# Performance work log

Hardware: AMD Instinct MI355X
Metric: run time of the kernel (lower is better)

## Reference

```python
import jax, jax.numpy as jnp
import numpy as np

B, S, CC, CF, E, H, NH = 16, 1024, 8, 8, 64, 1024, 16
DH = H // NH
VOCAB = 10000
EPS = 1e-5


def layer_norm(x, g, b):
    m = x.mean(-1, keepdims=True)
    v = x.var(-1, keepdims=True)
    return (x - m) / jnp.sqrt(v + EPS) * g + b


def setup_inputs():
    key = jax.random.key(0)
    ks = jax.random.split(key, 30)
    f32 = jnp.float32
    n = lambda k, shp, s=0.02: jax.random.normal(k, shp, f32) * s
    inp = {}
    inp['cate_x'] = jax.random.randint(ks[0], (B, S, CC), 0, VOCAB)
    inp['cont_x'] = jax.random.normal(ks[1], (B, S, CF), f32)
    inp['mask'] = jax.random.randint(ks[2], (B, S), 0, 2)
    # parameters
    inp['emb_table'] = n(ks[3], (VOCAB, E)).at[0].set(0.0)  # padding_idx=0
    inp['cate_W'] = n(ks[4], (CC * E, H)); inp['cate_b'] = jnp.zeros((H,), f32)
    inp['cate_ln_g'] = jnp.ones((H,), f32); inp['cate_ln_b'] = jnp.zeros((H,), f32)
    inp['bn_g'] = jnp.ones((CF,), f32); inp['bn_b'] = jnp.zeros((CF,), f32)
    inp['cont_W'] = n(ks[5], (CF, H)); inp['cont_b'] = jnp.zeros((H,), f32)
    inp['cont_ln_g'] = jnp.ones((H,), f32); inp['cont_ln_b'] = jnp.zeros((H,), f32)
    inp['comb_W'] = n(ks[6], (2 * H, H)); inp['comb_b'] = jnp.zeros((H,), f32)
    inp['comb_ln_g'] = jnp.ones((H,), f32); inp['comb_ln_b'] = jnp.zeros((H,), f32)
    inp['Wq'] = n(ks[7], (H, H)); inp['bq'] = jnp.zeros((H,), f32)
    inp['Wk'] = n(ks[8], (H, H)); inp['bk'] = jnp.zeros((H,), f32)
    inp['Wv'] = n(ks[9], (H, H)); inp['bv'] = jnp.zeros((H,), f32)
    inp['Wo'] = n(ks[10], (H, H)); inp['bo'] = jnp.zeros((H,), f32)
    return inp


def reference(cate_x, cont_x, mask, emb_table, cate_W, cate_b, cate_ln_g, cate_ln_b,
              bn_g, bn_b, cont_W, cont_b, cont_ln_g, cont_ln_b,
              comb_W, comb_b, comb_ln_g, comb_ln_b,
              Wq, bq, Wk, bk, Wv, bv, Wo, bo):
    # categorical path: embed -> flatten cols -> Linear+LN
    cate_emb = emb_table[cate_x].reshape(B, S, CC * E)
    cate_h = layer_norm(cate_emb @ cate_W + cate_b, cate_ln_g, cate_ln_b)
    # continuous path: BatchNorm1d over flattened (B*S, CF) with batch stats
    xf = cont_x.reshape(-1, CF)
    mu = xf.mean(0)
    var = xf.var(0)  # biased, as torch BN normalization
    xn = ((xf - mu) / jnp.sqrt(var + EPS) * bn_g + bn_b).reshape(B, S, CF)
    cont_h = layer_norm(xn @ cont_W + cont_b, cont_ln_g, cont_ln_b)
    # combine: ReLU -> Linear -> LN
    seq = jax.nn.relu(jnp.concatenate([cate_h, cont_h], axis=2))
    x = layer_norm(seq @ comb_W + comb_b, comb_ln_g, comb_ln_b)  # [B,S,H]
    # multi-head attention (dropout is identity in eval)
    Q = (x @ Wq + bq).reshape(B, S, NH, DH)
    K = (x @ Wk + bk).reshape(B, S, NH, DH)
    V = (x @ Wv + bv).reshape(B, S, NH, DH)
    scores = jnp.einsum('bqhd,bkhd->bhqk', Q, K) / np.sqrt(DH).astype(np.float32)
    # faithful to source: mask broadcast over the QUERY axis
    scores = jnp.where(mask[:, None, :, None] == 0, -1e7, scores)
    attn = jax.nn.softmax(scores, axis=-1)
    out = jnp.einsum('bhqk,bkhd->bqhd', attn, V).reshape(B, S, H)
    out = out @ Wo + bo
    return out[:, -1:, -1]  # [B,1]
```

## Files before the change

kernel.cpp:

```cpp
#include <hip/hip_runtime.h>
#include <hip/hip_bf16.h>
#include <math.h>

#define EPS 1e-5f

typedef unsigned short u16;
typedef __attribute__((ext_vector_type(8))) short bf16x8;
typedef __attribute__((ext_vector_type(4))) float f32x4;

__device__ __forceinline__ float b2f(u16 u) {
  union { unsigned int i; float f; } v; v.i = ((unsigned int)u) << 16; return v.f;
}
__device__ __forceinline__ u16 f2b(float f) {
  union { float f; unsigned int i; } v; v.f = f;
  unsigned int r = v.i + 0x7fff + ((v.i >> 16) & 1);
  return (u16)(r >> 16);
}

__device__ __forceinline__ void gload_lds16(const u16* g, u16* l) {
  __builtin_amdgcn_global_load_lds(
      (const __attribute__((address_space(1))) unsigned int*)g,
      (__attribute__((address_space(3))) unsigned int*)l, 16, 0, 0);
}

__global__ __launch_bounds__(256) void prep_k(
    const float* __restrict__ cx, float* __restrict__ part_bn,
    float* __restrict__ outacc,
    const float* __restrict__ emb, u16* __restrict__ embb,
    const float* __restrict__ cate_W, u16* __restrict__ cateWT) {
  __shared__ float shmem[64 * 65];
  const int bid = blockIdx.x, tid = threadIdx.x;

  if (bid == 0) {
    if (tid < 16) outacc[tid] = 0.f;
    return;
  }
  if (bid <= 64) {
    int pb = bid - 1;
    int gid = pb * 256 + tid;
    float4 a = ((const float4*)cx)[2 * gid];
    float4 b = ((const float4*)cx)[2 * gid + 1];
    float v[16];
    v[0] = a.x; v[1] = a.y; v[2] = a.z; v[3] = a.w;
    v[4] = b.x; v[5] = b.y; v[6] = b.z; v[7] = b.w;
#pragma unroll
    for (int i = 0; i < 8; ++i) v[8 + i] = v[i] * v[i];
#pragma unroll
    for (int off = 32; off; off >>= 1)
#pragma unroll
      for (int i = 0; i < 16; ++i) v[i] += __shfl_down(v[i], off);
    int l = tid & 63, wv_ = tid >> 6;
    if (l == 0)
#pragma unroll
      for (int i = 0; i < 16; ++i) shmem[wv_ * 16 + i] = v[i];
    __syncthreads();
    if (tid < 16)
      part_bn[pb * 16 + tid] = shmem[tid] + shmem[16 + tid] + shmem[32 + tid] + shmem[48 + tid];
    return;
  }
  if (bid <= 689) {
    int i = (bid - 65) * 256 + tid;
    if (i < 160000) {
      float4 v = ((const float4*)emb)[i];
      ushort4 u; u.x = f2b(v.x); u.y = f2b(v.y); u.z = f2b(v.z); u.w = f2b(v.w);
      ((ushort4*)embb)[i] = u;
    }
    return;
  }
  {
    int local = bid - 690;
    int n0 = (local & 15) * 64, k0 = (local >> 4) * 64;
    int c = tid & 63, r0 = tid >> 6;
#pragma unroll
    for (int i = 0; i < 16; ++i) {
      int r = r0 + i * 4;
      shmem[r * 65 + c] = cate_W[(size_t)(k0 + r) * 1024 + n0 + c];
    }
    __syncthreads();
#pragma unroll
    for (int i = 0; i < 16; ++i) {
      int r = r0 + i * 4;
      cateWT[(size_t)(n0 + r) * 512 + k0 + c] = f2b(shmem[c * 65 + r]);
    }
  }
}

template <int MODE>
__global__ __launch_bounds__(512) void gemm256(
    const u16* __restrict__ A0, const u16* __restrict__ A1,
    const int* __restrict__ idx, const u16* __restrict__ embb,
    const u16* __restrict__ BT, const float* __restrict__ bias,
    u16* __restrict__ C, int K) {
  __shared__ u16 As[2][2][8192];
  __shared__ u16 Bs[2][2][8192];
  __shared__ int sidx[MODE == 1 ? 2048 : 4];
  const int tid = threadIdx.x;
  const int bid = blockIdx.x;
  const int chunk = gridDim.x >> 3;
  const int swz = (bid & 7) * chunk + (bid >> 3);
  const int row0 = (swz >> 2) * 256;
  const int col0 = (swz & 3) * 256;

  const int rr8 = tid >> 3;
  const int p8  = tid & 7;
  const int sl  = p8 ^ (rr8 & 7);

  const int l   = tid & 63;
  const int w   = tid >> 6;
  const int wrh = w >> 2;
  const int wcq = w & 3;
  const int hb  = wcq >> 1;
  const int rbb = (wcq & 1) * 64;
  const int lr  = l & 15;
  const int lk  = l >> 4;

  f32x4 acc[8][4];
#pragma unroll
  for (int m = 0; m < 8; ++m)
#pragma unroll
    for (int n = 0; n < 4; ++n) acc[m][n] = (f32x4){0.f, 0.f, 0.f, 0.f};

  const int nt = K >> 6;
  const int nit = nt >> 1;

  if (MODE == 1) {
    *(int4*)&sidx[tid * 4] = *(const int4*)&idx[row0 * 8 + tid * 4];
    __syncthreads();
  }

  auto stageA = [&](int t, int h) {
    const int k0 = t << 6;
    const int buf = t & 1;
#pragma unroll
    for (int i = 0; i < 2; ++i) {
      const u16* asrc;
      if (MODE == 1) {
        int id = sidx[(h * 128 + i * 64 + rr8) * 8 + (k0 >> 6)];
        asrc = embb + (size_t)id * 64 + sl * 8;
      } else {
        int ar = row0 + h * 128 + i * 64 + rr8;
        const u16* base = (k0 < 1024) ? A0 : A1;
        asrc = base + (size_t)ar * 1024 + (k0 & 1023) + sl * 8;
      }
      gload_lds16(asrc, &As[buf][h][i * 4096 + tid * 8]);
    }
  };
  auto stageB = [&](int t, int h) {
    const int k0 = t << 6;
    const int buf = t & 1;
#pragma unroll
    for (int i = 0; i < 2; ++i) {
      int br = col0 + h * 128 + i * 64 + rr8;
      gload_lds16(BT + (size_t)br * K + k0 + sl * 8,
                  &Bs[buf][h][i * 4096 + tid * 8]);
    }
  };

  bf16x8 bfr[4][2];
  auto loadB = [&](int buf) {
#pragma unroll
    for (int n = 0; n < 4; ++n)
#pragma unroll
      for (int ks = 0; ks < 2; ++ks) {
        int rowb = rbb + n * 16 + lr;
        int ph = (ks * 4 + lk) ^ (lr & 7);
        bfr[n][ks] = *(const bf16x8*)&Bs[buf][hb][rowb * 64 + ph * 8];
      }
  };
  auto loadA = [&](bf16x8 (&af)[2][2], int buf, int q) {
#pragma unroll
    for (int mm = 0; mm < 2; ++mm)
#pragma unroll
      for (int ks = 0; ks < 2; ++ks) {
        int rowa = (q * 2 + mm) * 16 + lr;
        int ph = (ks * 4 + lk) ^ (lr & 7);
        af[mm][ks] = *(const bf16x8*)&As[buf][wrh][rowa * 64 + ph * 8];
      }
  };
  auto mfma_quad = [&](bf16x8 (&af)[2][2], int q) {
    __builtin_amdgcn_s_setprio(1);
#pragma unroll
    for (int ks = 0; ks < 2; ++ks)
#pragma unroll
      for (int mm = 0; mm < 2; ++mm)
#pragma unroll
        for (int n = 0; n < 4; ++n)
          acc[q * 2 + mm][n] = __builtin_amdgcn_mfma_f32_16x16x32_bf16(
              af[mm][ks], bfr[n][ks], acc[q * 2 + mm][n], 0, 0, 0);
    __builtin_amdgcn_s_setprio(0);
  };

  stageA(0, 0); stageA(0, 1);
  stageB(0, 0); stageB(0, 1);
  stageB(1, 0); stageB(1, 1);
  asm volatile("s_waitcnt vmcnt(4)" ::: "memory");
  __builtin_amdgcn_s_barrier();

  for (int it = 0; it < nit; ++it) {
    const int T = it * 2;
    const bool more = (T + 2 < nt);
    bf16x8 af[2][2];

    loadB(0); loadA(af, 0, 0);
    stageA(T + 1, 0);
    __builtin_amdgcn_s_barrier();
    asm volatile("s_waitcnt lgkmcnt(0)" ::: "memory");
    mfma_quad(af, 0);
    __builtin_amdgcn_s_barrier();
    loadA(af, 0, 1);
    stageA(T + 1, 1);
    __builtin_amdgcn_s_barrier();
    asm volatile("s_waitcnt lgkmcnt(0)" ::: "memory");
    mfma_quad(af, 1);
    __builtin_amdgcn_s_barrier();
    loadA(af, 0, 2);
    if (more) stageB(T + 2, 0);
    __builtin_amdgcn_s_barrier();
    asm volatile("s_waitcnt lgkmcnt(0)" ::: "memory");
    mfma_quad(af, 2);
    __builtin_amdgcn_s_barrier();
    loadA(af, 0, 3);
    if (more) stageB(T + 2, 1);
    __builtin_amdgcn_s_barrier();
    asm volatile("s_waitcnt lgkmcnt(0)" ::: "memory");
    mfma_quad(af, 3);
    if (more) asm volatile("s_waitcnt vmcnt(4)" ::: "memory");
    else      asm volatile("s_waitcnt vmcnt(0)" ::: "memory");
    __builtin_amdgcn_s_barrier();

    loadB(1); loadA(af, 1, 0);
    if (more) stageA(T + 2, 0);
    __builtin_amdgcn_s_barrier();
    asm volatile("s_waitcnt lgkmcnt(0)" ::: "memory");
    mfma_quad(af, 0);
    __builtin_amdgcn_s_barrier();
    loadA(af, 1, 1);
    if (more) stageA(T + 2, 1);
    __builtin_amdgcn_s_barrier();
    asm volatile("s_waitcnt lgkmcnt(0)" ::: "memory");
    mfma_quad(af, 1);
    __builtin_amdgcn_s_barrier();
    loadA(af, 1, 2);
    if (more) stageB(T + 3, 0);
    __builtin_amdgcn_s_barrier();
    asm volatile("s_waitcnt lgkmcnt(0)" ::: "memory");
    mfma_quad(af, 2);
    __builtin_amdgcn_s_barrier();
    loadA(af, 1, 3);
    if (more) stageB(T + 3, 1);
    __builtin_amdgcn_s_barrier();
    asm volatile("s_waitcnt lgkmcnt(0)" ::: "memory");
    mfma_quad(af, 3);
    if (it + 1 < nit) {
      asm volatile("s_waitcnt vmcnt(4)" ::: "memory");
      __builtin_amdgcn_s_barrier();
    }
  }

  float bv_[4];
#pragma unroll
  for (int n = 0; n < 4; ++n) bv_[n] = bias[col0 + wcq * 64 + n * 16 + lr];
#pragma unroll
  for (int m = 0; m < 8; ++m) {
#pragma unroll
    for (int n = 0; n < 4; ++n) {
      int cc = col0 + wcq * 64 + n * 16 + lr;
#pragma unroll
      for (int q4 = 0; q4 < 4; ++q4) {
        int rr = row0 + wrh * 128 + m * 16 + lk * 4 + q4;
        C[(size_t)rr * 1024 + cc] = f2b(acc[m][n][q4] + bv_[n]);
      }
    }
  }
}

__device__ __forceinline__ void ln_body(u16* __restrict__ buf,
                                        const float* __restrict__ g,
                                        const float* __restrict__ b, int relu,
                                        int blk, int tid) {
  int lane = tid & 63, wave = tid >> 6;
  size_t row = (size_t)blk * 4 + wave;
  u16* p = buf + row * 1024 + lane * 16;
  uint4 u0 = *(uint4*)p;
  uint4 u1 = *(uint4*)(p + 8);
  float x[16];
#pragma unroll
  for (int i = 0; i < 4; ++i) {
    unsigned int w0 = ((unsigned int*)&u0)[i];
    unsigned int w1 = ((unsigned int*)&u1)[i];
    x[2 * i]     = b2f((u16)(w0 & 0xffff));
    x[2 * i + 1] = b2f((u16)(w0 >> 16));
    x[8 + 2 * i]     = b2f((u16)(w1 & 0xffff));
    x[8 + 2 * i + 1] = b2f((u16)(w1 >> 16));
  }
  float s = 0.f, s2 = 0.f;
#pragma unroll
  for (int i = 0; i < 16; ++i) { s += x[i]; s2 += x[i] * x[i]; }
#pragma unroll
  for (int off = 32; off; off >>= 1) { s += __shfl_xor(s, off); s2 += __shfl_xor(s2, off); }
  float mean = s * (1.f / 1024.f);
  float var = s2 * (1.f / 1024.f) - mean * mean;
  float rs = rsqrtf(var + EPS);
  float y[16];
#pragma unroll
  for (int q = 0; q < 4; ++q) {
    float4 gv = *(const float4*)(g + lane * 16 + q * 4);
    float4 bv = *(const float4*)(b + lane * 16 + q * 4);
    y[4 * q]     = (x[4 * q]     - mean) * rs * gv.x + bv.x;
    y[4 * q + 1] = (x[4 * q + 1] - mean) * rs * gv.y + bv.y;
    y[4 * q + 2] = (x[4 * q + 2] - mean) * rs * gv.z + bv.z;
    y[4 * q + 3] = (x[4 * q + 3] - mean) * rs * gv.w + bv.w;
  }
  if (relu)
#pragma unroll
    for (int i = 0; i < 16; ++i) y[i] = fmaxf(y[i], 0.f);
  uint4 o0, o1;
#pragma unroll
  for (int i = 0; i < 4; ++i) {
    ((unsigned int*)&o0)[i] = (unsigned int)f2b(y[2 * i]) | ((unsigned int)f2b(y[2 * i + 1]) << 16);
    ((unsigned int*)&o1)[i] = (unsigned int)f2b(y[8 + 2 * i]) | ((unsigned int)f2b(y[8 + 2 * i + 1]) << 16);
  }
  *(uint4*)p = o0;
  *(uint4*)(p + 8) = o1;
}

__global__ __launch_bounds__(256) void ln_k(u16* __restrict__ buf,
                                            const float* __restrict__ g,
                                            const float* __restrict__ b, int relu) {
  ln_body(buf, g, b, relu, blockIdx.x, threadIdx.x);
}

__device__ __forceinline__ void cont_body(const float* __restrict__ cx,
                                          const float* __restrict__ part_bn,
                                          const float* __restrict__ bn_g,
                                          const float* __restrict__ bn_b,
                                          const float* __restrict__ W,
                                          const float* __restrict__ cb,
                                          const float* __restrict__ g,
                                          const float* __restrict__ bb,
                                          u16* __restrict__ out,
                                          int row0, int tid) {
  __shared__ float sp[4][16];
  __shared__ float tt[16];
  __shared__ float ab[2][8];
  __shared__ float xn[8][8];
  __shared__ float rr1[4][8], rr2[4][8];

  if (tid < 64) {
    int f = tid & 15, qd = tid >> 4;
    float s = 0.f;
    for (int j = qd * 16; j < qd * 16 + 16; ++j) s += part_bn[j * 16 + f];
    sp[qd][f] = s;
  }
  __syncthreads();
  if (tid < 16) tt[tid] = sp[0][tid] + sp[1][tid] + sp[2][tid] + sp[3][tid];
  __syncthreads();
  if (tid < 8) {
    float mu = tt[tid] * (1.f / 16384.f);
    float var = tt[8 + tid] * (1.f / 16384.f) - mu * mu;
    float a = rsqrtf(var + EPS) * bn_g[tid];
    ab[0][tid] = a;
    ab[1][tid] = bn_b[tid] - mu * a;
  }
  __syncthreads();
  if (tid < 64) {
    int r = tid >> 3, f = tid & 7;
    xn[r][f] = ab[0][f] * cx[(row0 + r) * 8 + f] + ab[1][f];
  }
  __syncthreads();

  int c = tid * 4;
  float4 cbv = *(const float4*)(cb + c);
  float acc[8][4];
#pragma unroll
  for (int r = 0; r < 8; ++r) {
    acc[r][0] = cbv.x; acc[r][1] = cbv.y; acc[r][2] = cbv.z; acc[r][3] = cbv.w;
  }
  for (int k = 0; k < 8; ++k) {
    float4 w4 = *(const float4*)(W + k * 1024 + c);
#pragma unroll
    for (int r = 0; r < 8; ++r) {
      float xv = xn[r][k];
      acc[r][0] = fmaf(xv, w4.x, acc[r][0]);
      acc[r][1] = fmaf(xv, w4.y, acc[r][1]);
      acc[r][2] = fmaf(xv, w4.z, acc[r][2]);
      acc[r][3] = fmaf(xv, w4.w, acc[r][3]);
    }
  }
  float s1[8], s2[8];
#pragma unroll
  for (int r = 0; r < 8; ++r) {
    s1[r] = acc[r][0] + acc[r][1] + acc[r][2] + acc[r][3];
    s2[r] = acc[r][0] * acc[r][0] + acc[r][1] * acc[r][1] +
            acc[r][2] * acc[r][2] + acc[r][3] * acc[r][3];
  }
#pragma unroll
  for (int off = 32; off; off >>= 1)
#pragma unroll
    for (int r = 0; r < 8; ++r) {
      s1[r] += __shfl_down(s1[r], off);
      s2[r] += __shfl_down(s2[r], off);
    }
  int lane = tid & 63, wv = tid >> 6;
  if (lane == 0)
#pragma unroll
    for (int r = 0; r < 8; ++r) { rr1[wv][r] = s1[r]; rr2[wv][r] = s2[r]; }
  __syncthreads();
  float4 gv = *(const float4*)(g + c);
  float4 bv = *(const float4*)(bb + c);
#pragma unroll
  for (int r = 0; r < 8; ++r) {
    float ss = rr1[0][r] + rr1[1][r] + rr1[2][r] + rr1[3][r];
    float qq = rr2[0][r] + rr2[1][r] + rr2[2][r] + rr2[3][r];
    float mean = ss * (1.f / 1024.f);
    float var = qq * (1.f / 1024.f) - mean * mean;
    float rs = rsqrtf(var + EPS);
    float y0 = fmaxf((acc[r][0] - mean) * rs * gv.x + bv.x, 0.f);
    float y1 = fmaxf((acc[r][1] - mean) * rs * gv.y + bv.y, 0.f);
    float y2 = fmaxf((acc[r][2] - mean) * rs * gv.z + bv.z, 0.f);
    float y3 = fmaxf((acc[r][3] - mean) * rs * gv.w + bv.w, 0.f);
    ushort4 o; o.x = f2b(y0); o.y = f2b(y1); o.z = f2b(y2); o.w = f2b(y3);
    *(ushort4*)(out + (size_t)(row0 + r) * 1024 + c) = o;
  }
}

__global__ __launch_bounds__(256) void mid_k(
    u16* __restrict__ X1, const float* __restrict__ cate_g,
    const float* __restrict__ cate_bb,
    const float* __restrict__ comb_W, u16* __restrict__ combWT,
    const float* __restrict__ Wv, const float* __restrict__ Wo,
    u16* __restrict__ wvob_hi, u16* __restrict__ wvob_lo,
    float* __restrict__ woc,
    const float* __restrict__ cx, const float* __restrict__ part_bn,
    const float* __restrict__ bn_g, const float* __restrict__ bn_b,
    const float* __restrict__ cont_W, const float* __restrict__ cont_b,
    const float* __restrict__ cont_g, const float* __restrict__ cont_bb,
    u16* __restrict__ X2) {
  __shared__ float shmem[64 * 65];
  const int bid = blockIdx.x, tid = threadIdx.x;
  if (bid < 4096) {
    ln_body(X1, cate_g, cate_bb, 1, bid, tid);
    return;
  }
  if (bid < 4608) {
    int local = bid - 4096;
    int n0 = (local & 15) * 64, k0 = (local >> 4) * 64;
    int c = tid & 63, r0 = tid >> 6;
#pragma unroll
    for (int i = 0; i < 16; ++i) {
      int r = r0 + i * 4;
      shmem[r * 65 + c] = comb_W[(size_t)(k0 + r) * 1024 + n0 + c];
    }
    __syncthreads();
#pragma unroll
    for (int i = 0; i < 16; ++i) {
      int r = r0 + i * 4;
      combWT[(size_t)(n0 + r) * 2048 + k0 + c] = f2b(shmem[c * 65 + r]);
    }
    return;
  }
  if (bid < 4672) {
    int local = bid - 4608;
    int h = local >> 2, jc = local & 3;
    if (tid < 64) shmem[tid] = Wo[(size_t)(h * 64 + tid) * 1024 + 1023];
    __syncthreads();
    if (jc == 0 && tid < 64) woc[h * 64 + tid] = shmem[tid];
    int j = jc * 256 + tid;
    const float* vr = Wv + (size_t)j * 1024 + h * 64;
    float s = 0.f;
    for (int d4 = 0; d4 < 64; d4 += 4) {
      float4 w4 = *(const float4*)(vr + d4);
      s = fmaf(w4.x, shmem[d4], s);
      s = fmaf(w4.y, shmem[d4 + 1], s);
      s = fmaf(w4.z, shmem[d4 + 2], s);
      s = fmaf(w4.w, shmem[d4 + 3], s);
    }
    u16 hi = f2b(s);
    float lo = s - b2f(hi);
    wvob_hi[h * 1024 + j] = hi;
    wvob_lo[h * 1024 + j] = f2b(lo);
    return;
  }
  {
    int row0 = (bid - 4672) * 8;
    cont_body(cx, part_bn, bn_g, bn_b, cont_W, cont_b, cont_g, cont_bb, X2,
              row0, tid);
  }
}

__global__ __launch_bounds__(256) void qproj_k(const u16* __restrict__ x,
                                               const float* __restrict__ Wq,
                                               const float* __restrict__ bq,
                                               float* __restrict__ q) {
  __shared__ u16 xs[16][1024];
  __shared__ float part[16][16][16];
  int tid = threadIdx.x;
  for (int i = tid; i < 4096; i += 256) {
    int b = i >> 8, off = (i & 255) * 4;
    *(ushort4*)&xs[b][off] =
        *(const ushort4*)(x + ((size_t)(b * 1024 + 1023)) * 1024 + off);
  }
  __syncthreads();
  int c = tid & 15;
  int col = blockIdx.x * 16 + c;
  int kq = tid >> 4;
  float acc[16];
#pragma unroll
  for (int b = 0; b < 16; ++b) acc[b] = 0.f;
  for (int k = kq * 64; k < kq * 64 + 64; ++k) {
    float wv = Wq[(size_t)k * 1024 + col];
#pragma unroll
    for (int b = 0; b < 16; ++b) acc[b] = fmaf(b2f(xs[b][k]), wv, acc[b]);
  }
#pragma unroll
  for (int b = 0; b < 16; ++b) part[kq][b][c] = acc[b];
  __syncthreads();
  if (tid < 256) {
    int b = tid >> 4, cc = tid & 15;
    float s = 0.f;
#pragma unroll
    for (int j = 0; j < 16; ++j) s += part[j][b][cc];
    q[b * 1024 + blockIdx.x * 16 + cc] = s + bq[blockIdx.x * 16 + cc];
  }
}

__global__ __launch_bounds__(256) void kq_k(const float* __restrict__ Wk,
                                            const float* __restrict__ bk,
                                            const float* __restrict__ q,
                                            u16* __restrict__ qtb,
                                            float* __restrict__ bkq) {
  int h = blockIdx.x >> 2, jc = blockIdx.x & 3;
  int tid = threadIdx.x;
  __shared__ float Qs[16][64];
  for (int i = tid; i < 1024; i += 256) {
    int b = i >> 6, d = i & 63;
    Qs[b][d] = q[b * 1024 + h * 64 + d];
  }
  __syncthreads();
  int j = jc * 256 + tid;
  float acc[16];
#pragma unroll
  for (int b = 0; b < 16; ++b) acc[b] = 0.f;
  const float* wr = Wk + (size_t)j * 1024 + h * 64;
  for (int d4 = 0; d4 < 64; d4 += 4) {
    float4 w4 = *(const float4*)(wr + d4);
#pragma unroll
    for (int b = 0; b < 16; ++b) {
      acc[b] = fmaf(w4.x, Qs[b][d4], acc[b]);
      acc[b] = fmaf(w4.y, Qs[b][d4 + 1], acc[b]);
      acc[b] = fmaf(w4.z, Qs[b][d4 + 2], acc[b]);
      acc[b] = fmaf(w4.w, Qs[b][d4 + 3], acc[b]);
    }
  }
#pragma unroll
  for (int b = 0; b < 16; ++b) qtb[((size_t)b * 16 + h) * 1024 + j] = f2b(acc[b]);
  if (jc == 0 && tid < 16) {
    int b = tid;
    float s = 0.f;
    for (int d = 0; d < 64; ++d) s = fmaf(bk[h * 64 + d], Qs[b][d], s);
    bkq[b * 16 + h] = s;
  }
}

__global__ __launch_bounds__(256) void score_k(const u16* __restrict__ x,
                                               const u16* __restrict__ qtb,
                                               const float* __restrict__ bkq,
                                               const int* __restrict__ mask,
                                               const u16* __restrict__ whi,
                                               const u16* __restrict__ wlo,
                                               float* __restrict__ sc,
                                               float* __restrict__ y) {
  int b = blockIdx.x >> 4, kc = blockIdx.x & 15;
  int tid = threadIdx.x;
  int l = tid & 63, w = tid >> 6;
  int keybase = kc * 64 + w * 16;
  int lr = l & 15, ls = l >> 4;
  int masked = (mask[b * 1024 + 1023] == 0);

  f32x4 acc = (f32x4){0.f, 0.f, 0.f, 0.f};
  f32x4 acy = (f32x4){0.f, 0.f, 0.f, 0.f};
  const u16* xb = x + (size_t)b * 1024 * 1024;
  const u16* qb = qtb + (size_t)b * 16 * 1024;
  for (int k0 = 0; k0 < 1024; k0 += 32) {
    bf16x8 bfr = *(const bf16x8*)&qb[(size_t)lr * 1024 + k0 + ls * 8];
    bf16x8 bh  = *(const bf16x8*)&whi[(size_t)lr * 1024 + k0 + ls * 8];
    bf16x8 bl  = *(const bf16x8*)&wlo[(size_t)lr * 1024 + k0 + ls * 8];
    bf16x8 afr = *(const bf16x8*)&xb[(size_t)(keybase + lr) * 1024 + k0 + ls * 8];
    acc = __builtin_amdgcn_mfma_f32_16x16x32_bf16(afr, bfr, acc, 0, 0, 0);
    acy = __builtin_amdgcn_mfma_f32_16x16x32_bf16(afr, bh, acy, 0, 0, 0);
    acy = __builtin_amdgcn_mfma_f32_16x16x32_bf16(afr, bl, acy, 0, 0, 0);
  }
  int h = lr;
  float bq_ = bkq[b * 16 + h];
#pragma unroll
  for (int q = 0; q < 4; ++q) {
    int key = keybase + ls * 4 + q;
    float v = masked ? 0.f : (acc[q] + bq_) * 0.125f;
    sc[((size_t)b * 16 + h) * 1024 + key] = v;
    y[((size_t)b * 16 + h) * 1024 + key] = acy[q];
  }
}

__global__ __launch_bounds__(256) void fin_k(const float* __restrict__ sc,
                                             const float* __restrict__ y,
                                             float* __restrict__ outacc) {
  int bh = blockIdx.x, tid = threadIdx.x;
  float4 v = ((const float4*)(sc + (size_t)bh * 1024))[tid];
  float m = fmaxf(fmaxf(v.x, v.y), fmaxf(v.z, v.w));
#pragma unroll
  for (int off = 32; off; off >>= 1) m = fmaxf(m, __shfl_down(m, off));
  __shared__ float rm[4], rs_[4], rd_[4];
  int lane = tid & 63, wv = tid >> 6;
  if (lane == 0) rm[wv] = m;
  __syncthreads();
  m = fmaxf(fmaxf(rm[0], rm[1]), fmaxf(rm[2], rm[3]));
  float e0 = expf(v.x - m), e1 = expf(v.y - m), e2 = expf(v.z - m), e3 = expf(v.w - m);
  float4 yv = ((const float4*)(y + (size_t)bh * 1024))[tid];
  float s = e0 + e1 + e2 + e3;
  float d = e0 * yv.x + e1 * yv.y + e2 * yv.z + e3 * yv.w;
#pragma unroll
  for (int off = 32; off; off >>= 1) {
    s += __shfl_down(s, off);
    d += __shfl_down(d, off);
  }
  if (lane == 0) { rs_[wv] = s; rd_[wv] = d; }
  __syncthreads();
  if (tid == 0) {
    float Z = rs_[0] + rs_[1] + rs_[2] + rs_[3];
    float D = rd_[0] + rd_[1] + rd_[2] + rd_[3];
    atomicAdd(&outacc[bh >> 4], D / Z);
  }
}

__global__ __launch_bounds__(256) void bfinal_k(const float* __restrict__ outacc,
                                                const float* __restrict__ bv,
                                                const float* __restrict__ woc,
                                                const float* __restrict__ bo,
                                                float* __restrict__ out) {
  int tid = threadIdx.x;
  float s = 0.f;
  for (int i = tid; i < 1024; i += 256) s = fmaf(bv[i], woc[i], s);
#pragma unroll
  for (int off = 32; off; off >>= 1) s += __shfl_down(s, off);
  __shared__ float r[4];
  int lane = tid & 63, wv = tid >> 6;
  if (lane == 0) r[wv] = s;
  __syncthreads();
  float bc = r[0] + r[1] + r[2] + r[3] + bo[1023];
  if (tid < 16) out[tid] = outacc[tid] + bc;
}

extern "C" void kernel_launch(void* const* d_in, const int* in_sizes, int n_in,
                              void* d_out, int out_size, void* d_ws, size_t ws_size,
                              hipStream_t stream) {
  const int*   cate_x  = (const int*)d_in[0];
  const float* cont_x  = (const float*)d_in[1];
  const int*   mask    = (const int*)d_in[2];
  const float* emb     = (const float*)d_in[3];
  const float* cate_W  = (const float*)d_in[4];
  const float* cate_b  = (const float*)d_in[5];
  const float* cate_g  = (const float*)d_in[6];
  const float* cate_bb = (const float*)d_in[7];
  const float* bn_g    = (const float*)d_in[8];
  const float* bn_b    = (const float*)d_in[9];
  const float* cont_W  = (const float*)d_in[10];
  const float* cont_b  = (const float*)d_in[11];
  const float* cont_g  = (const float*)d_in[12];
  const float* cont_bb = (const float*)d_in[13];
  const float* Wq = (const float*)d_in[18]; const float* bq = (const float*)d_in[19];
  const float* Wk = (const float*)d_in[20]; const float* bk = (const float*)d_in[21];
  const float* Wv = (const float*)d_in[22]; const float* bv = (const float*)d_in[23];
  const float* Wo = (const float*)d_in[24]; const float* bo = (const float*)d_in[25];
  const float* comb_W  = (const float*)d_in[14];
  const float* comb_b  = (const float*)d_in[15];
  const float* comb_g  = (const float*)d_in[16];
  const float* comb_bb = (const float*)d_in[17];
  float* out = (float*)d_out;

  char* w = (char*)d_ws;
  float* stats   = (float*)w;
  float* outacc  = stats + 16;
  float* part_bn = (float*)(w + 256);
  float* qbuf    = (float*)(w + 8192);
  u16* embb      = (u16*)(w + 131328);
  u16* cateWT    = (u16*)(w + 1411328);
  u16* combWT    = (u16*)(w + 2459904);
  float* sc      = (float*)(w + 6654208);
  u16*   qtb     = (u16*)(w + 7702784);
  float* bkq     = (float*)(w + 8292608);
  float* ybuf    = (float*)(w + 8388608);
  u16* wvob_hi   = (u16*)(w + 9437184);
  u16* wvob_lo   = (u16*)(w + 9469952);
  float* woc     = (float*)(w + 9502720);
  u16* X1        = (u16*)(w + 10848512);
  u16* X2        = X1 + (size_t)16777216;
  u16* xb        = X2 + (size_t)16777216;

  prep_k<<<818, 256, 0, stream>>>(cont_x, part_bn, outacc, emb, embb,
                                  cate_W, cateWT);

  gemm256<1><<<256, 512, 0, stream>>>(nullptr, nullptr, cate_x, embb, cateWT,
                                      cate_b, X1, 512);
  mid_k<<<6720, 256, 0, stream>>>(X1, cate_g, cate_bb, comb_W, combWT, Wv, Wo,
                                  wvob_hi, wvob_lo, woc, cont_x, part_bn, bn_g,
                                  bn_b, cont_W, cont_b, cont_g, cont_bb, X2);
  gemm256<2><<<256, 512, 0, stream>>>(X1, X2, nullptr, nullptr, combWT,
                                      comb_b, xb, 2048);
  ln_k<<<4096, 256, 0, stream>>>(xb, comb_g, comb_bb, 0);

  qproj_k<<<64, 256, 0, stream>>>(xb, Wq, bq, qbuf);
  kq_k<<<64, 256, 0, stream>>>(Wk, bk, qbuf, qtb, bkq);
  score_k<<<256, 256, 0, stream>>>(xb, qtb, bkq, mask, wvob_hi, wvob_lo, sc, ybuf);
  fin_k<<<256, 256, 0, stream>>>(sc, ybuf, outacc);
  bfinal_k<<<1, 256, 0, stream>>>(outacc, bv, woc, bo, out);
}
```

Measured before the change: 198.7 us.

## Fuse attention tail kernels into one cooperative kernel with grid syncs

The five small tail kernels (q projection, K·q, score MFMA, softmax finalize, bias final) are merged into a single cooperative kernel of 256 blocks, with grid.sync() between stages. This removes four kernel launch boundaries and their inter-kernel gaps on a tail that is latency-dominated. In exchange it adds grid-wide barrier costs and a cooperative launch, and the combined shared memory (~45KB per block) may limit residency.

Result: slower. 297.7 us (+49.8%).

```diff
diff --git a/kernel.cpp b/kernel.cpp
--- a/kernel.cpp
+++ b/kernel.cpp
@@ -1,6 +1,9 @@
 #include <hip/hip_runtime.h>
 #include <hip/hip_bf16.h>
+#include <hip/hip_cooperative_groups.h>
 #include <math.h>
+
+namespace cg = cooperative_groups;
 
 #define EPS 1e-5f
 
@@ -488,166 +491,163 @@
   }
 }
 
-__global__ __launch_bounds__(256) void qproj_k(const u16* __restrict__ x,
-                                               const float* __restrict__ Wq,
-                                               const float* __restrict__ bq,
-                                               float* __restrict__ q) {
-  __shared__ u16 xs[16][1024];
-  __shared__ float part[16][16][16];
-  int tid = threadIdx.x;
-  for (int i = tid; i < 4096; i += 256) {
-    int b = i >> 8, off = (i & 255) * 4;
-    *(ushort4*)&xs[b][off] =
-        *(const ushort4*)(x + ((size_t)(b * 1024 + 1023)) * 1024 + off);
-  }
-  __syncthreads();
-  int c = tid & 15;
-  int col = blockIdx.x * 16 + c;
-  int kq = tid >> 4;
-  float acc[16];
-#pragma unroll
-  for (int b = 0; b < 16; ++b) acc[b] = 0.f;
-  for (int k = kq * 64; k < kq * 64 + 64; ++k) {
-    float wv = Wq[(size_t)k * 1024 + col];
-#pragma unroll
-    for (int b = 0; b < 16; ++b) acc[b] = fmaf(b2f(xs[b][k]), wv, acc[b]);
-  }
-#pragma unroll
-  for (int b = 0; b < 16; ++b) part[kq][b][c] = acc[b];
-  __syncthreads();
-  if (tid < 256) {
-    int b = tid >> 4, cc = tid & 15;
+__global__ __launch_bounds__(256) void tail_k(
+    const u16* __restrict__ x,
+    const float* __restrict__ Wq, const float* __restrict__ bq,
+    float* __restrict__ q,
+    const float* __restrict__ Wk, const float* __restrict__ bk,
+    u16* __restrict__ qtb, float* __restrict__ bkq,
+    const int* __restrict__ mask,
+    const u16* __restrict__ whi, const u16* __restrict__ wlo,
+    float* __restrict__ sc, float* __restrict__ y,
+    float* __restrict__ outacc,
+    const float* __restrict__ bv, const float* __restrict__ woc,
+    const float* __restrict__ bo, float* __restrict__ out) {
+  cg::grid_group grid = cg::this_grid();
+  const int bid = blockIdx.x, tid = threadIdx.x;
+
+  if (bid < 64) {
+    __shared__ u16 xs[16][1024];
+    __shared__ float part[16][16][16];
+    for (int i = tid; i < 4096; i += 256) {
+      int b = i >> 8, off = (i & 255) * 4;
+      *(ushort4*)&xs[b][off] =
+          *(const ushort4*)(x + ((size_t)(b * 1024 + 1023)) * 1024 + off);
+    }
+    __syncthreads();
+    int c = tid & 15;
+    int col = bid * 16 + c;
+    int kq = tid >> 4;
+    float acc[16];
+#pragma unroll
+    for (int b = 0; b < 16; ++b) acc[b] = 0.f;
+    for (int k = kq * 64; k < kq * 64 + 64; ++k) {
+      float wv = Wq[(size_t)k * 1024 + col];
+#pragma unroll
+      for (int b = 0; b < 16; ++b) acc[b] = fmaf(b2f(xs[b][k]), wv, acc[b]);
+    }
+#pragma unroll
+    for (int b = 0; b < 16; ++b) part[kq][b][c] = acc[b];
+    __syncthreads();
+    {
+      int b = tid >> 4, cc = tid & 15;
+      float s = 0.f;
+#pragma unroll
+      for (int j = 0; j < 16; ++j) s += part[j][b][cc];
+      q[b * 1024 + bid * 16 + cc] = s + bq[bid * 16 + cc];
+    }
+  }
+  grid.sync();
+
+  if (bid < 64) {
+    int h = bid >> 2, jc = bid & 3;
+    __shared__ float Qs[16][64];
+    for (int i = tid; i < 1024; i += 256) {
+      int b = i >> 6, d = i & 63;
+      Qs[b][d] = q[b * 1024 + h * 64 + d];
+    }
+    __syncthreads();
+    int j = jc * 256 + tid;
+    float acc[16];
+#pragma unroll
+    for (int b = 0; b < 16; ++b) acc[b] = 0.f;
+    const float* wr = Wk + (size_t)j * 1024 + h * 64;
+    for (int d4 = 0; d4 < 64; d4 += 4) {
+      float4 w4 = *(const float4*)(wr + d4);
+#pragma unroll
+      for (int b = 0; b < 16; ++b) {
+        acc[b] = fmaf(w4.x, Qs[b][d4], acc[b]);
+        acc[b] = fmaf(w4.y, Qs[b][d4 + 1], acc[b]);
+        acc[b] = fmaf(w4.z, Qs[b][d4 + 2], acc[b]);
+        acc[b] = fmaf(w4.w, Qs[b][d4 + 3], acc[b]);
+      }
+    }
+#pragma unroll
+    for (int b = 0; b < 16; ++b) qtb[((size_t)b * 16 + h) * 1024 + j] = f2b(acc[b]);
+    if (jc == 0 && tid < 16) {
+      int b = tid;
+      float s = 0.f;
+      for (int d = 0; d < 64; ++d) s = fmaf(bk[h * 64 + d], Qs[b][d], s);
+      bkq[b * 16 + h] = s;
+    }
+  }
+  grid.sync();
+
+  {
+    int b = bid >> 4, kc = bid & 15;
+    int l = tid & 63, w = tid >> 6;
+    int keybase = kc * 64 + w * 16;
+    int lr = l & 15, ls = l >> 4;
+    int masked = (mask[b * 1024 + 1023] == 0);
+
+    f32x4 acc = (f32x4){0.f, 0.f, 0.f, 0.f};
+    f32x4 acy = (f32x4){0.f, 0.f, 0.f, 0.f};
+    const u16* xb = x + (size_t)b * 1024 * 1024;
+    const u16* qb = qtb + (size_t)b * 16 * 1024;
+    for (int k0 = 0; k0 < 1024; k0 += 32) {
+      bf16x8 bfr = *(const bf16x8*)&qb[(size_t)lr * 1024 + k0 + ls * 8];
+      bf16x8 bh  = *(const bf16x8*)&whi[(size_t)lr * 1024 + k0 + ls * 8];
+      bf16x8 bl  = *(const bf16x8*)&wlo[(size_t)lr * 1024 + k0 + ls * 8];
+      bf16x8 afr = *(const bf16x8*)&xb[(size_t)(keybase + lr) * 1024 + k0 + ls * 8];
+      acc = __builtin_amdgcn_mfma_f32_16x16x32_bf16(afr, bfr, acc, 0, 0, 0);
+      acy = __builtin_amdgcn_mfma_f32_16x16x32_bf16(afr, bh, acy, 0, 0, 0);
+      acy = __builtin_amdgcn_mfma_f32_16x16x32_bf16(afr, bl, acy, 0, 0, 0);
+    }
+    int h = lr;
+    float bq_ = bkq[b * 16 + h];
+#pragma unroll
+    for (int qq = 0; qq < 4; ++qq) {
+      int key = keybase + ls * 4 + qq;
+      float v = masked ? 0.f : (acc[qq] + bq_) * 0.125f;
+      sc[((size_t)b * 16 + h) * 1024 + key] = v;
+      y[((size_t)b * 16 + h) * 1024 + key] = acy[qq];
+    }
+  }
+  grid.sync();
+
+  {
+    int bh = bid;
+    float4 v = ((const float4*)(sc + (size_t)bh * 1024))[tid];
+    float m = fmaxf(fmaxf(v.x, v.y), fmaxf(v.z, v.w));
+#pragma unroll
+    for (int off = 32; off; off >>= 1) m = fmaxf(m, __shfl_down(m, off));
+    __shared__ float rm[4], rs_[4], rd_[4];
+    int lane = tid & 63, wv = tid >> 6;
+    if (lane == 0) rm[wv] = m;
+    __syncthreads();
+    m = fmaxf(fmaxf(rm[0], rm[1]), fmaxf(rm[2], rm[3]));
+    float e0 = expf(v.x - m), e1 = expf(v.y - m);
+    float e2 = expf(v.z - m), e3 = expf(v.w - m);
+    float4 yv = ((const float4*)(y + (size_t)bh * 1024))[tid];
+    float s = e0 + e1 + e2 + e3;
+    float d = e0 * yv.x + e1 * yv.y + e2 * yv.z + e3 * yv.w;
+#pragma unroll
+    for (int off = 32; off; off >>= 1) {
+      s += __shfl_down(s, off);
+      d += __shfl_down(d, off);
+    }
+    if (lane == 0) { rs_[wv] = s; rd_[wv] = d; }
+    __syncthreads();
+    if (tid == 0) {
+      float Z = rs_[0] + rs_[1] + rs_[2] + rs_[3];
+      float D = rd_[0] + rd_[1] + rd_[2] + rd_[3];
+      atomicAdd(&outacc[bh >> 4], D / Z);
+    }
+  }
+  grid.sync();
+
+  if (bid == 0) {
     float s = 0.f;
-#pragma unroll
-    for (int j = 0; j < 16; ++j) s += part[j][b][cc];
-    q[b * 1024 + blockIdx.x * 16 + cc] = s + bq[blockIdx.x * 16 + cc];
-  }
-}
-
-__global__ __launch_bounds__(256) void kq_k(const float* __restrict__ Wk,
-                                            const float* __restrict__ bk,
-                                            const float* __restrict__ q,
-                                            u16* __restrict__ qtb,
-                                            float* __restrict__ bkq) {
-  int h = blockIdx.x >> 2, jc = blockIdx.x & 3;
-  int tid = threadIdx.x;
-  __shared__ float Qs[16][64];
-  for (int i = tid; i < 1024; i += 256) {
-    int b = i >> 6, d = i & 63;
-    Qs[b][d] = q[b * 1024 + h * 64 + d];
-  }
-  __syncthreads();
-  int j = jc * 256 + tid;
-  float acc[16];
-#pragma unroll
-  for (int b = 0; b < 16; ++b) acc[b] = 0.f;
-  const float* wr = Wk + (size_t)j * 1024 + h * 64;
-  for (int d4 = 0; d4 < 64; d4 += 4) {
-    float4 w4 = *(const float4*)(wr + d4);
-#pragma unroll
-    for (int b = 0; b < 16; ++b) {
-      acc[b] = fmaf(w4.x, Qs[b][d4], acc[b]);
-      acc[b] = fmaf(w4.y, Qs[b][d4 + 1], acc[b]);
-      acc[b] = fmaf(w4.z, Qs[b][d4 + 2], acc[b]);
-      acc[b] = fmaf(w4.w, Qs[b][d4 + 3], acc[b]);
-    }
-  }
-#pragma unroll
-  for (int b = 0; b < 16; ++b) qtb[((size_t)b * 16 + h) * 1024 + j] = f2b(acc[b]);
-  if (jc == 0 && tid < 16) {
-    int b = tid;
-    float s = 0.f;
-    for (int d = 0; d < 64; ++d) s = fmaf(bk[h * 64 + d], Qs[b][d], s);
-    bkq[b * 16 + h] = s;
-  }
-}
-
-__global__ __launch_bounds__(256) void score_k(const u16* __restrict__ x,
-                                               const u16* __restrict__ qtb,
-                                               const float* __restrict__ bkq,
-                                               const int* __restrict__ mask,
-                                               const u16* __restrict__ whi,
-                                               const u16* __restrict__ wlo,
-                                               float* __restrict__ sc,
-                                               float* __restrict__ y) {
-  int b = blockIdx.x >> 4, kc = blockIdx.x & 15;
-  int tid = threadIdx.x;
-  int l = tid & 63, w = tid >> 6;
-  int keybase = kc * 64 + w * 16;
-  int lr = l & 15, ls = l >> 4;
-  int masked = (mask[b * 1024 + 1023] == 0);
-
-  f32x4 acc = (f32x4){0.f, 0.f, 0.f, 0.f};
-  f32x4 acy = (f32x4){0.f, 0.f, 0.f, 0.f};
-  const u16* xb = x + (size_t)b * 1024 * 1024;
-  const u16* qb = qtb + (size_t)b * 16 * 1024;
-  for (int k0 = 0; k0 < 1024; k0 += 32) {
-    bf16x8 bfr = *(const bf16x8*)&qb[(size_t)lr * 1024 + k0 + ls * 8];
-    bf16x8 bh  = *(const bf16x8*)&whi[(size_t)lr * 1024 + k0 + ls * 8];
-    bf16x8 bl  = *(const bf16x8*)&wlo[(size_t)lr * 1024 + k0 + ls * 8];
-    bf16x8 afr = *(const bf16x8*)&xb[(size_t)(keybase + lr) * 1024 + k0 + ls * 8];
-    acc = __builtin_amdgcn_mfma_f32_16x16x32_bf16(afr, bfr, acc, 0, 0, 0);
-    acy = __builtin_amdgcn_mfma_f32_16x16x32_bf16(afr, bh, acy, 0, 0, 0);
-    acy = __builtin_amdgcn_mfma_f32_16x16x32_bf16(afr, bl, acy, 0, 0, 0);
-  }
-  int h = lr;
-  float bq_ = bkq[b * 16 + h];
-#pragma unroll
-  for (int q = 0; q < 4; ++q) {
-    int key = keybase + ls * 4 + q;
-    float v = masked ? 0.f : (acc[q] + bq_) * 0.125f;
-    sc[((size_t)b * 16 + h) * 1024 + key] = v;
-    y[((size_t)b * 16 + h) * 1024 + key] = acy[q];
-  }
-}
-
-__global__ __launch_bounds__(256) void fin_k(const float* __restrict__ sc,
-                                             const float* __restrict__ y,
-                                             float* __restrict__ outacc) {
-  int bh = blockIdx.x, tid = threadIdx.x;
-  float4 v = ((const float4*)(sc + (size_t)bh * 1024))[tid];
-  float m = fmaxf(fmaxf(v.x, v.y), fmaxf(v.z, v.w));
-#pragma unroll
-  for (int off = 32; off; off >>= 1) m = fmaxf(m, __shfl_down(m, off));
-  __shared__ float rm[4], rs_[4], rd_[4];
-  int lane = tid & 63, wv = tid >> 6;
-  if (lane == 0) rm[wv] = m;
-  __syncthreads();
-  m = fmaxf(fmaxf(rm[0], rm[1]), fmaxf(rm[2], rm[3]));
-  float e0 = expf(v.x - m), e1 = expf(v.y - m), e2 = expf(v.z - m), e3 = expf(v.w - m);
-  float4 yv = ((const float4*)(y + (size_t)bh * 1024))[tid];
-  float s = e0 + e1 + e2 + e3;
-  float d = e0 * yv.x + e1 * yv.y + e2 * yv.z + e3 * yv.w;
-#pragma unroll
-  for (int off = 32; off; off >>= 1) {
-    s += __shfl_down(s, off);
-    d += __shfl_down(d, off);
-  }
-  if (lane == 0) { rs_[wv] = s; rd_[wv] = d; }
-  __syncthreads();
-  if (tid == 0) {
-    float Z = rs_[0] + rs_[1] + rs_[2] + rs_[3];
-    float D = rd_[0] + rd_[1] + rd_[2] + rd_[3];
-    atomicAdd(&outacc[bh >> 4], D / Z);
-  }
-}
-
-__global__ __launch_bounds__(256) void bfinal_k(const float* __restrict__ outacc,
-                                                const float* __restrict__ bv,
-                                                const float* __restrict__ woc,
-                                                const float* __restrict__ bo,
-                                                float* __restrict__ out) {
-  int tid = threadIdx.x;
-  float s = 0.f;
-  for (int i = tid; i < 1024; i += 256) s = fmaf(bv[i], woc[i], s);
-#pragma unroll
-  for (int off = 32; off; off >>= 1) s += __shfl_down(s, off);
-  __shared__ float r[4];
-  int lane = tid & 63, wv = tid >> 6;
-  if (lane == 0) r[wv] = s;
-  __syncthreads();
-  float bc = r[0] + r[1] + r[2] + r[3] + bo[1023];
-  if (tid < 16) out[tid] = outacc[tid] + bc;
+    for (int i = tid; i < 1024; i += 256) s = fmaf(bv[i], woc[i], s);
+#pragma unroll
+    for (int off = 32; off; off >>= 1) s += __shfl_down(s, off);
+    __shared__ float r[4];
+    int lane = tid & 63, wv = tid >> 6;
+    if (lane == 0) r[wv] = s;
+    __syncthreads();
+    float bc = r[0] + r[1] + r[2] + r[3] + bo[1023];
+    if (tid < 16) out[tid] = outacc[tid] + bc;
+  }
 }
 
 extern "C" void kernel_launch(void* const* d_in, const int* in_sizes, int n_in,
@@ -708,9 +708,15 @@
                                       comb_b, xb, 2048);
   ln_k<<<4096, 256, 0, stream>>>(xb, comb_g, comb_bb, 0);
 
-  qproj_k<<<64, 256, 0, stream>>>(xb, Wq, bq, qbuf);
-  kq_k<<<64, 256, 0, stream>>>(Wk, bk, qbuf, qtb, bkq);
-  score_k<<<256, 256, 0, stream>>>(xb, qtb, bkq, mask, wvob_hi, wvob_lo, sc, ybuf);
-  fin_k<<<256, 256, 0, stream>>>(sc, ybuf, outacc);
-  bfinal_k<<<1, 256, 0, stream>>>(outacc, bv, woc, bo, out);
-}
+  {
+    const u16* xcb = xb;
+    void* targs[] = {
+        (void*)&xcb, (void*)&Wq, (void*)&bq, (void*)&qbuf,
+        (void*)&Wk, (void*)&bk, (void*)&qtb, (void*)&bkq,
+        (void*)&mask, (void*)&wvob_hi, (void*)&wvob_lo,
+        (void*)&sc, (void*)&ybuf, (void*)&outacc,
+        (void*)&bv, (void*)&woc, (void*)&bo, (void*)&out};
+    hipLaunchCooperativeKernel((const void*)tail_k, dim3(256), dim3(256),
+                               targs, 0, stream);
+  }
+}
```

## Fold final LayerNorm into downstream projections via per-row stats from GEMM epilogue

Applied to the files above, without the earlier changes.

The standalone comb LayerNorm pass over the 16M-element xb buffer is removed. The comb GEMM epilogue now emits per-row partial sums and sums of squares, and a small kernel turns them into mean and rstd. Gamma and beta are folded algebraically into the K-side query vectors and the V·Wo weights, and correction terms are applied per key in score_k. This removes one full read-modify-write of the activation buffer and a launch, at the cost of extra reductions, atomics and some precision risk from computing variance as E[x²]-mean² on bf16 outputs.

Result: faster. 192.4 us (-3.2%).

```diff
diff --git a/kernel.cpp b/kernel.cpp
--- a/kernel.cpp
+++ b/kernel.cpp
@@ -25,7 +25,7 @@
 
 __global__ __launch_bounds__(256) void prep_k(
     const float* __restrict__ cx, float* __restrict__ part_bn,
-    float* __restrict__ outacc,
+    float* __restrict__ outacc, float* __restrict__ Sall,
     const float* __restrict__ emb, u16* __restrict__ embb,
     const float* __restrict__ cate_W, u16* __restrict__ cateWT) {
   __shared__ float shmem[64 * 65];
@@ -33,6 +33,7 @@
 
   if (bid == 0) {
     if (tid < 16) outacc[tid] = 0.f;
+    for (int i = tid; i < 544; i += 256) Sall[i] = 0.f;
     return;
   }
   if (bid <= 64) {
@@ -90,7 +91,7 @@
     const u16* __restrict__ A0, const u16* __restrict__ A1,
     const int* __restrict__ idx, const u16* __restrict__ embb,
     const u16* __restrict__ BT, const float* __restrict__ bias,
-    u16* __restrict__ C, int K) {
+    u16* __restrict__ C, int K, float* __restrict__ pstat) {
   __shared__ u16 As[2][2][8192];
   __shared__ u16 Bs[2][2][8192];
   __shared__ int sidx[MODE == 1 ? 2048 : 4];
@@ -272,6 +273,54 @@
       }
     }
   }
+
+  if (MODE == 2) {
+    __syncthreads();
+    float* sst = (float*)&As[0][0][0];
+#pragma unroll
+    for (int m = 0; m < 8; ++m) {
+#pragma unroll
+      for (int q4 = 0; q4 < 4; ++q4) {
+        float p1 = 0.f, p2 = 0.f;
+#pragma unroll
+        for (int n = 0; n < 4; ++n) {
+          float v = acc[m][n][q4] + bv_[n];
+          p1 += v; p2 += v * v;
+        }
+#pragma unroll
+        for (int off = 1; off < 16; off <<= 1) {
+          p1 += __shfl_xor(p1, off);
+          p2 += __shfl_xor(p2, off);
+        }
+        if (lr == 0) {
+          int rl = wrh * 128 + m * 16 + lk * 4 + q4;
+          sst[(rl * 4 + wcq) * 2 + 0] = p1;
+          sst[(rl * 4 + wcq) * 2 + 1] = p2;
+        }
+      }
+    }
+    __syncthreads();
+    if (tid < 256) {
+      int rl = tid;
+      float s1 = sst[rl * 8] + sst[rl * 8 + 2] + sst[rl * 8 + 4] + sst[rl * 8 + 6];
+      float s2 = sst[rl * 8 + 1] + sst[rl * 8 + 3] + sst[rl * 8 + 5] + sst[rl * 8 + 7];
+      size_t row = (size_t)(row0 + rl);
+      pstat[(row * 4 + (col0 >> 8)) * 2 + 0] = s1;
+      pstat[(row * 4 + (col0 >> 8)) * 2 + 1] = s2;
+    }
+  }
+}
+
+__global__ __launch_bounds__(256) void stat_k(const float* __restrict__ pstat,
+                                              float* __restrict__ stats) {
+  int row = blockIdx.x * 256 + threadIdx.x;
+  const float* p = pstat + (size_t)row * 8;
+  float s1 = p[0] + p[2] + p[4] + p[6];
+  float s2 = p[1] + p[3] + p[5] + p[7];
+  float mean = s1 * (1.f / 1024.f);
+  float var = s2 * (1.f / 1024.f) - mean * mean;
+  stats[row * 2] = mean;
+  stats[row * 2 + 1] = rsqrtf(var + EPS);
 }
 
 __device__ __forceinline__ void ln_body(u16* __restrict__ buf,
@@ -322,12 +371,6 @@
   }
   *(uint4*)p = o0;
   *(uint4*)(p + 8) = o1;
-}
-
-__global__ __launch_bounds__(256) void ln_k(u16* __restrict__ buf,
-                                            const float* __restrict__ g,
-                                            const float* __restrict__ b, int relu) {
-  ln_body(buf, g, b, relu, blockIdx.x, threadIdx.x);
 }
 
 __device__ __forceinline__ void cont_body(const float* __restrict__ cx,
@@ -429,8 +472,9 @@
     const float* __restrict__ cate_bb,
     const float* __restrict__ comb_W, u16* __restrict__ combWT,
     const float* __restrict__ Wv, const float* __restrict__ Wo,
+    const float* __restrict__ comb_g, const float* __restrict__ comb_bbv,
     u16* __restrict__ wvob_hi, u16* __restrict__ wvob_lo,
-    float* __restrict__ woc,
+    float* __restrict__ woc, float* __restrict__ Swg, float* __restrict__ Swb,
     const float* __restrict__ cx, const float* __restrict__ part_bn,
     const float* __restrict__ bn_g, const float* __restrict__ bn_b,
     const float* __restrict__ cont_W, const float* __restrict__ cont_b,
@@ -475,10 +519,25 @@
       s = fmaf(w4.z, shmem[d4 + 2], s);
       s = fmaf(w4.w, shmem[d4 + 3], s);
     }
-    u16 hi = f2b(s);
-    float lo = s - b2f(hi);
+    float sg_ = s * comb_g[j];
+    u16 hi = f2b(sg_);
+    float lo = sg_ - b2f(hi);
     wvob_hi[h * 1024 + j] = hi;
     wvob_lo[h * 1024 + j] = f2b(lo);
+    float swgp = sg_;
+    float swbp = s * comb_bbv[j];
+#pragma unroll
+    for (int off = 32; off; off >>= 1) {
+      swgp += __shfl_down(swgp, off);
+      swbp += __shfl_down(swbp, off);
+    }
+    int lane = tid & 63, wv = tid >> 6;
+    if (lane == 0) { shmem[64 + wv] = swgp; shmem[68 + wv] = swbp; }
+    __syncthreads();
+    if (tid == 0) {
+      atomicAdd(&Swg[h], shmem[64] + shmem[65] + shmem[66] + shmem[67]);
+      atomicAdd(&Swb[h], shmem[68] + shmem[69] + shmem[70] + shmem[71]);
+    }
     return;
   }
   {
@@ -489,16 +548,35 @@
 }
 
 __global__ __launch_bounds__(256) void qproj_k(const u16* __restrict__ x,
+                                               const float* __restrict__ stats,
+                                               const float* __restrict__ g,
+                                               const float* __restrict__ bb,
                                                const float* __restrict__ Wq,
                                                const float* __restrict__ bq,
                                                float* __restrict__ q) {
   __shared__ u16 xs[16][1024];
   __shared__ float part[16][16][16];
+  __shared__ float sm[16], sr[16];
   int tid = threadIdx.x;
+  if (tid < 16) {
+    size_t row = (size_t)tid * 1024 + 1023;
+    sm[tid] = stats[row * 2];
+    sr[tid] = stats[row * 2 + 1];
+  }
+  __syncthreads();
   for (int i = tid; i < 4096; i += 256) {
     int b = i >> 8, off = (i & 255) * 4;
-    *(ushort4*)&xs[b][off] =
+    ushort4 u =
         *(const ushort4*)(x + ((size_t)(b * 1024 + 1023)) * 1024 + off);
+    float4 gv = *(const float4*)(g + off);
+    float4 bv = *(const float4*)(bb + off);
+    float m = sm[b], r = sr[b];
+    ushort4 o;
+    o.x = f2b((b2f(u.x) - m) * r * gv.x + bv.x);
+    o.y = f2b((b2f(u.y) - m) * r * gv.y + bv.y);
+    o.z = f2b((b2f(u.z) - m) * r * gv.z + bv.z);
+    o.w = f2b((b2f(u.w) - m) * r * gv.w + bv.w);
+    *(ushort4*)&xs[b][off] = o;
   }
   __syncthreads();
   int c = tid & 15;
@@ -515,7 +593,7 @@
 #pragma unroll
   for (int b = 0; b < 16; ++b) part[kq][b][c] = acc[b];
   __syncthreads();
-  if (tid < 256) {
+  {
     int b = tid >> 4, cc = tid & 15;
     float s = 0.f;
 #pragma unroll
@@ -527,11 +605,16 @@
 __global__ __launch_bounds__(256) void kq_k(const float* __restrict__ Wk,
                                             const float* __restrict__ bk,
                                             const float* __restrict__ q,
+                                            const float* __restrict__ g,
+                                            const float* __restrict__ bb,
                                             u16* __restrict__ qtb,
-                                            float* __restrict__ bkq) {
+                                            float* __restrict__ bkq,
+                                            float* __restrict__ Sg,
+                                            float* __restrict__ Sb) {
   int h = blockIdx.x >> 2, jc = blockIdx.x & 3;
   int tid = threadIdx.x;
   __shared__ float Qs[16][64];
+  __shared__ float rg[4][16], rb[4][16];
   for (int i = tid; i < 1024; i += 256) {
     int b = i >> 6, d = i & 63;
     Qs[b][d] = q[b * 1024 + h * 64 + d];
@@ -552,8 +635,32 @@
       acc[b] = fmaf(w4.w, Qs[b][d4 + 3], acc[b]);
     }
   }
-#pragma unroll
-  for (int b = 0; b < 16; ++b) qtb[((size_t)b * 16 + h) * 1024 + j] = f2b(acc[b]);
+  float gj = g[j], bbj = bb[j];
+  float sgp[16], sbp[16];
+#pragma unroll
+  for (int b = 0; b < 16; ++b) {
+    u16 qg = f2b(acc[b] * gj);
+    qtb[((size_t)b * 16 + h) * 1024 + j] = qg;
+    sgp[b] = b2f(qg);
+    sbp[b] = acc[b] * bbj;
+  }
+#pragma unroll
+  for (int off = 32; off; off >>= 1)
+#pragma unroll
+    for (int b = 0; b < 16; ++b) {
+      sgp[b] += __shfl_down(sgp[b], off);
+      sbp[b] += __shfl_down(sbp[b], off);
+    }
+  int lane = tid & 63, wv = tid >> 6;
+  if (lane == 0)
+#pragma unroll
+    for (int b = 0; b < 16; ++b) { rg[wv][b] = sgp[b]; rb[wv][b] = sbp[b]; }
+  __syncthreads();
+  if (tid < 16) {
+    int b = tid;
+    atomicAdd(&Sg[b * 16 + h], rg[0][b] + rg[1][b] + rg[2][b] + rg[3][b]);
+    atomicAdd(&Sb[b * 16 + h], rb[0][b] + rb[1][b] + rb[2][b] + rb[3][b]);
+  }
   if (jc == 0 && tid < 16) {
     int b = tid;
     float s = 0.f;
@@ -562,14 +669,14 @@
   }
 }
 
-__global__ __launch_bounds__(256) void score_k(const u16* __restrict__ x,
-                                               const u16* __restrict__ qtb,
-                                               const float* __restrict__ bkq,
-                                               const int* __restrict__ mask,
-                                               const u16* __restrict__ whi,
-                                               const u16* __restrict__ wlo,
-                                               float* __restrict__ sc,
-                                               float* __restrict__ y) {
+__global__ __launch_bounds__(256) void score_k(
+    const u16* __restrict__ x, const u16* __restrict__ qtb,
+    const float* __restrict__ bkq, const int* __restrict__ mask,
+    const u16* __restrict__ whi, const u16* __restrict__ wlo,
+    const float* __restrict__ stats,
+    const float* __restrict__ Sg, const float* __restrict__ Sb,
+    const float* __restrict__ Swg, const float* __restrict__ Swb,
+    float* __restrict__ sc, float* __restrict__ y) {
   int b = blockIdx.x >> 4, kc = blockIdx.x & 15;
   int tid = threadIdx.x;
   int l = tid & 63, w = tid >> 6;
@@ -591,13 +698,22 @@
     acy = __builtin_amdgcn_mfma_f32_16x16x32_bf16(afr, bl, acy, 0, 0, 0);
   }
   int h = lr;
-  float bq_ = bkq[b * 16 + h];
+  float bq_  = bkq[b * 16 + h];
+  float Sgv  = Sg[b * 16 + h];
+  float Sbv  = Sb[b * 16 + h];
+  float Swgv = Swg[h];
+  float Swbv = Swb[h];
 #pragma unroll
   for (int q = 0; q < 4; ++q) {
     int key = keybase + ls * 4 + q;
-    float v = masked ? 0.f : (acc[q] + bq_) * 0.125f;
+    size_t row = (size_t)b * 1024 + key;
+    float mean = stats[row * 2];
+    float rs   = stats[row * 2 + 1];
+    float sraw = rs * acc[q] - rs * mean * Sgv + Sbv + bq_;
+    float v = masked ? 0.f : sraw * 0.125f;
     sc[((size_t)b * 16 + h) * 1024 + key] = v;
-    y[((size_t)b * 16 + h) * 1024 + key] = acy[q];
+    y[((size_t)b * 16 + h) * 1024 + key] =
+        rs * acy[q] - rs * mean * Swgv + Swbv;
   }
 }
 
@@ -678,8 +794,8 @@
   float* out = (float*)d_out;
 
   char* w = (char*)d_ws;
-  float* stats   = (float*)w;
-  float* outacc  = stats + 16;
+  float* stats0  = (float*)w;
+  float* outacc  = stats0 + 16;
   float* part_bn = (float*)(w + 256);
   float* qbuf    = (float*)(w + 8192);
   u16* embb      = (u16*)(w + 131328);
@@ -692,25 +808,34 @@
   u16* wvob_hi   = (u16*)(w + 9437184);
   u16* wvob_lo   = (u16*)(w + 9469952);
   float* woc     = (float*)(w + 9502720);
+  float* pstat   = (float*)(w + 9506816);
+  float* lstats  = (float*)(w + 10031104);
+  float* Sall    = (float*)(w + 10162176);
+  float* Sg      = Sall;
+  float* Sb      = Sall + 256;
+  float* Swg     = Sall + 512;
+  float* Swb     = Sall + 528;
   u16* X1        = (u16*)(w + 10848512);
   u16* X2        = X1 + (size_t)16777216;
   u16* xb        = X2 + (size_t)16777216;
 
-  prep_k<<<818, 256, 0, stream>>>(cont_x, part_bn, outacc, emb, embb,
+  prep_k<<<818, 256, 0, stream>>>(cont_x, part_bn, outacc, Sall, emb, embb,
                                   cate_W, cateWT);
 
   gemm256<1><<<256, 512, 0, stream>>>(nullptr, nullptr, cate_x, embb, cateWT,
-                                      cate_b, X1, 512);
+                                      cate_b, X1, 512, nullptr);
   mid_k<<<6720, 256, 0, stream>>>(X1, cate_g, cate_bb, comb_W, combWT, Wv, Wo,
-                                  wvob_hi, wvob_lo, woc, cont_x, part_bn, bn_g,
-                                  bn_b, cont_W, cont_b, cont_g, cont_bb, X2);
+                                  comb_g, comb_bb, wvob_hi, wvob_lo, woc, Swg,
+                                  Swb, cont_x, part_bn, bn_g, bn_b, cont_W,
+                                  cont_b, cont_g, cont_bb, X2);
   gemm256<2><<<256, 512, 0, stream>>>(X1, X2, nullptr, nullptr, combWT,
-                                      comb_b, xb, 2048);
-  ln_k<<<4096, 256, 0, stream>>>(xb, comb_g, comb_bb, 0);
-
-  qproj_k<<<64, 256, 0, stream>>>(xb, Wq, bq, qbuf);
-  kq_k<<<64, 256, 0, stream>>>(Wk, bk, qbuf, qtb, bkq);
-  score_k<<<256, 256, 0, stream>>>(xb, qtb, bkq, mask, wvob_hi, wvob_lo, sc, ybuf);
+                                      comb_b, xb, 2048, pstat);
+  stat_k<<<64, 256, 0, stream>>>(pstat, lstats);
+
+  qproj_k<<<64, 256, 0, stream>>>(xb, lstats, comb_g, comb_bb, Wq, bq, qbuf);
+  kq_k<<<64, 256, 0, stream>>>(Wk, bk, qbuf, comb_g, comb_bb, qtb, bkq, Sg, Sb);
+  score_k<<<256, 256, 0, stream>>>(xb, qtb, bkq, mask, wvob_hi, wvob_lo,
+                                   lstats, Sg, Sb, Swg, Swb, sc, ybuf);
   fin_k<<<256, 256, 0, stream>>>(sc, ybuf, outacc);
   bfinal_k<<<1, 256, 0, stream>>>(outacc, bv, woc, bo, out);
 }
```
